# Performance work log

Hardware: AMD Instinct MI355X
Metric: run time of the kernel (lower is better)

## Reference

```python
import jax, jax.numpy as jnp
import numpy as np

B, C, T = 32, 256, 4096

def setup_inputs() -> dict:
    key = jax.random.key(0)
    k1, k2 = jax.random.split(key)
    x = jax.random.normal(k1, (B, C, T), dtype=jnp.float32)
    gamma = jax.random.normal(k2, (1,), dtype=jnp.float32)
    return {"x": x, "gamma": gamma}

def reference(x, gamma):
    # energy[b,i,j] = <x[b,i,:], x[b,j,:]>  -> (B, C, C)
    energy = jnp.einsum('bit,bjt->bij', x, x)
    # max-subtract trick: softmax over (rowmax - energy)
    energy_new = jnp.max(energy, axis=-1, keepdims=True) - energy
    attention = jax.nn.softmax(energy_new, axis=-1)
    # out[b,i,t] = sum_j attention[b,i,j] * x[b,j,t]
    out = jnp.einsum('bij,bjt->bit', attention, x)
    return gamma * out + x
```

## Files before the change

### kernel.cpp

```cpp
#include <hip/hip_runtime.h>
#include <hip/hip_bf16.h>

#define BATCH 32
#define CDIM  256
#define TDIM  4096

using short8  = __attribute__((ext_vector_type(8))) short;
using floatx4 = __attribute__((ext_vector_type(4))) float;

__device__ __forceinline__ unsigned f2bf(float f) {
  unsigned u = __float_as_uint(f);
  return (u + 0x7fffu + ((u >> 16) & 1u)) >> 16;
}
__device__ __forceinline__ unsigned cvt_pk_bf16(float a, float b) {
  return f2bf(a) | (f2bf(b) << 16);
}
__device__ __forceinline__ float bf_lo(unsigned u) { return __uint_as_float(u << 16); }
__device__ __forceinline__ float bf_hi(unsigned u) { return __uint_as_float(u & 0xffff0000u); }

__global__ __launch_bounds__(512, 1)
void gram_kernel(const float* __restrict__ x,
                 float* __restrict__ E1, float* __restrict__ E2) {
  __shared__ __align__(16) short hI[128 * 64];
  __shared__ __align__(16) short lI[128 * 64];
  __shared__ __align__(16) short hJ[64 * 64];

  const int tid = threadIdx.x;
  const int bx  = blockIdx.x;

  const int s   = bx & 7;
  const int seq = bx >> 3;
  const int b   = s + ((seq >> 3) << 3);
  const int job = seq & 7;
  const int i0  = (job >> 2) << 7;
  const int j0  = (job & 3) << 6;

  const float* xb = x + ((size_t)b << 20);

  const bool isJ   = tid >= 256;
  const int  irow  = tid >> 1;
  const int  ihalf = tid & 1;
  const int  jrow  = (tid & 255) >> 2;
  const int  jq    = tid & 3;

  const float* pS = isJ
      ? xb + (size_t)(j0 + jrow) * TDIM + (jq << 4)
      : xb + (size_t)(i0 + irow) * TDIM + (ihalf << 5);

  floatx4 acc1[2][2], acc2[2][2];
#pragma unroll
  for (int m = 0; m < 2; ++m)
#pragma unroll
    for (int n = 0; n < 2; ++n) {
      acc1[m][n] = {0.f, 0.f, 0.f, 0.f};
      acc2[m][n] = {0.f, 0.f, 0.f, 0.f};
    }

  const int lane = tid & 63;
  const int w    = tid >> 6;
  const int wib  = (w >> 1) << 5;
  const int wjb  = (w & 1) << 5;
  const int fr   = lane & 15;
  const int q    = lane >> 4;
  const int f7   = fr & 7;

  const int g0 = ((q)     ^ f7) << 3;
  const int g1 = ((q + 4) ^ f7) << 3;
  const int a0 = (wib + fr) << 6;
  const int a1 = (wib + 16 + fr) << 6;
  const int b0 = (wjb + fr) << 6;
  const int b1 = (wjb + 16 + fr) << 6;

  float4 r0, r1, r2, r3, r4, r5, r6, r7;
  r0 = ((const float4*)pS)[0]; r1 = ((const float4*)pS)[1];
  r2 = ((const float4*)pS)[2]; r3 = ((const float4*)pS)[3];
  if (!isJ) {
    r4 = ((const float4*)pS)[4]; r5 = ((const float4*)pS)[5];
    r6 = ((const float4*)pS)[6]; r7 = ((const float4*)pS)[7];
  }

  for (int ks = 0; ks < TDIM / 64; ++ks) {
    unsigned h0 = cvt_pk_bf16(r0.x, r0.y), h1 = cvt_pk_bf16(r0.z, r0.w);
    unsigned h2 = cvt_pk_bf16(r1.x, r1.y), h3 = cvt_pk_bf16(r1.z, r1.w);
    unsigned h4 = cvt_pk_bf16(r2.x, r2.y), h5 = cvt_pk_bf16(r2.z, r2.w);
    unsigned h6 = cvt_pk_bf16(r3.x, r3.y), h7 = cvt_pk_bf16(r3.z, r3.w);
    unsigned h8, h9, hA, hB, hC, hD, hE, hF;
    unsigned l0, l1, l2, l3, l4, l5, l6, l7, l8, l9, lA, lB, lC, lD, lE, lF;
    if (!isJ) {
      h8 = cvt_pk_bf16(r4.x, r4.y); h9 = cvt_pk_bf16(r4.z, r4.w);
      hA = cvt_pk_bf16(r5.x, r5.y); hB = cvt_pk_bf16(r5.z, r5.w);
      hC = cvt_pk_bf16(r6.x, r6.y); hD = cvt_pk_bf16(r6.z, r6.w);
      hE = cvt_pk_bf16(r7.x, r7.y); hF = cvt_pk_bf16(r7.z, r7.w);
      l0 = cvt_pk_bf16(r0.x - bf_lo(h0), r0.y - bf_hi(h0));
      l1 = cvt_pk_bf16(r0.z - bf_lo(h1), r0.w - bf_hi(h1));
      l2 = cvt_pk_bf16(r1.x - bf_lo(h2), r1.y - bf_hi(h2));
      l3 = cvt_pk_bf16(r1.z - bf_lo(h3), r1.w - bf_hi(h3));
      l4 = cvt_pk_bf16(r2.x - bf_lo(h4), r2.y - bf_hi(h4));
      l5 = cvt_pk_bf16(r2.z - bf_lo(h5), r2.w - bf_hi(h5));
      l6 = cvt_pk_bf16(r3.x - bf_lo(h6), r3.y - bf_hi(h6));
      l7 = cvt_pk_bf16(r3.z - bf_lo(h7), r3.w - bf_hi(h7));
      l8 = cvt_pk_bf16(r4.x - bf_lo(h8), r4.y - bf_hi(h8));
      l9 = cvt_pk_bf16(r4.z - bf_lo(h9), r4.w - bf_hi(h9));
      lA = cvt_pk_bf16(r5.x - bf_lo(hA), r5.y - bf_hi(hA));
      lB = cvt_pk_bf16(r5.z - bf_lo(hB), r5.w - bf_hi(hB));
      lC = cvt_pk_bf16(r6.x - bf_lo(hC), r6.y - bf_hi(hC));
      lD = cvt_pk_bf16(r6.z - bf_lo(hD), r6.w - bf_hi(hD));
      lE = cvt_pk_bf16(r7.x - bf_lo(hE), r7.y - bf_hi(hE));
      lF = cvt_pk_bf16(r7.z - bf_lo(hF), r7.w - bf_hi(hF));
    }

    __syncthreads();
    if (!isJ) {
      const int rb = irow << 6;
      const int s7 = irow & 7;
      const int gb = ihalf << 2;
      *(uint4*)&hI[rb + (((gb + 0) ^ s7) << 3)] = make_uint4(h0, h1, h2, h3);
      *(uint4*)&hI[rb + (((gb + 1) ^ s7) << 3)] = make_uint4(h4, h5, h6, h7);
      *(uint4*)&hI[rb + (((gb + 2) ^ s7) << 3)] = make_uint4(h8, h9, hA, hB);
      *(uint4*)&hI[rb + (((gb + 3) ^ s7) << 3)] = make_uint4(hC, hD, hE, hF);
      *(uint4*)&lI[rb + (((gb + 0) ^ s7) << 3)] = make_uint4(l0, l1, l2, l3);
      *(uint4*)&lI[rb + (((gb + 1) ^ s7) << 3)] = make_uint4(l4, l5, l6, l7);
      *(uint4*)&lI[rb + (((gb + 2) ^ s7) << 3)] = make_uint4(l8, l9, lA, lB);
      *(uint4*)&lI[rb + (((gb + 3) ^ s7) << 3)] = make_uint4(lC, lD, lE, lF);
    } else {
      const int rb = jrow << 6;
      const int s7 = jrow & 7;
      const int gb = jq << 1;
      *(uint4*)&hJ[rb + (((gb + 0) ^ s7) << 3)] = make_uint4(h0, h1, h2, h3);
      *(uint4*)&hJ[rb + (((gb + 1) ^ s7) << 3)] = make_uint4(h4, h5, h6, h7);
    }
    __syncthreads();

    if (ks < TDIM / 64 - 1) {
      pS += 64;
      r0 = ((const float4*)pS)[0]; r1 = ((const float4*)pS)[1];
      r2 = ((const float4*)pS)[2]; r3 = ((const float4*)pS)[3];
      if (!isJ) {
        r4 = ((const float4*)pS)[4]; r5 = ((const float4*)pS)[5];
        r6 = ((const float4*)pS)[6]; r7 = ((const float4*)pS)[7];
      }
    }

    {
      short8 Ah0 = *(const short8*)&hI[a0 + g0];
      short8 Ah1 = *(const short8*)&hI[a1 + g0];
      short8 Al0 = *(const short8*)&lI[a0 + g0];
      short8 Al1 = *(const short8*)&lI[a1 + g0];
      short8 Bh0 = *(const short8*)&hJ[b0 + g0];
      short8 Bh1 = *(const short8*)&hJ[b1 + g0];
      acc1[0][0] = __builtin_amdgcn_mfma_f32_16x16x32_bf16(Ah0, Bh0, acc1[0][0], 0, 0, 0);
      acc1[0][1] = __builtin_amdgcn_mfma_f32_16x16x32_bf16(Ah0, Bh1, acc1[0][1], 0, 0, 0);
      acc1[1][0] = __builtin_amdgcn_mfma_f32_16x16x32_bf16(Ah1, Bh0, acc1[1][0], 0, 0, 0);
      acc1[1][1] = __builtin_amdgcn_mfma_f32_16x16x32_bf16(Ah1, Bh1, acc1[1][1], 0, 0, 0);
      acc2[0][0] = __builtin_amdgcn_mfma_f32_16x16x32_bf16(Al0, Bh0, acc2[0][0], 0, 0, 0);
      acc2[0][1] = __builtin_amdgcn_mfma_f32_16x16x32_bf16(Al0, Bh1, acc2[0][1], 0, 0, 0);
      acc2[1][0] = __builtin_amdgcn_mfma_f32_16x16x32_bf16(Al1, Bh0, acc2[1][0], 0, 0, 0);
      acc2[1][1] = __builtin_amdgcn_mfma_f32_16x16x32_bf16(Al1, Bh1, acc2[1][1], 0, 0, 0);
    }
    {
      short8 Ah0 = *(const short8*)&hI[a0 + g1];
      short8 Ah1 = *(const short8*)&hI[a1 + g1];
      short8 Al0 = *(const short8*)&lI[a0 + g1];
      short8 Al1 = *(const short8*)&lI[a1 + g1];
      short8 Bh0 = *(const short8*)&hJ[b0 + g1];
      short8 Bh1 = *(const short8*)&hJ[b1 + g1];
      acc1[0][0] = __builtin_amdgcn_mfma_f32_16x16x32_bf16(Ah0, Bh0, acc1[0][0], 0, 0, 0);
      acc1[0][1] = __builtin_amdgcn_mfma_f32_16x16x32_bf16(Ah0, Bh1, acc1[0][1], 0, 0, 0);
      acc1[1][0] = __builtin_amdgcn_mfma_f32_16x16x32_bf16(Ah1, Bh0, acc1[1][0], 0, 0, 0);
      acc1[1][1] = __builtin_amdgcn_mfma_f32_16x16x32_bf16(Ah1, Bh1, acc1[1][1], 0, 0, 0);
      acc2[0][0] = __builtin_amdgcn_mfma_f32_16x16x32_bf16(Al0, Bh0, acc2[0][0], 0, 0, 0);
      acc2[0][1] = __builtin_amdgcn_mfma_f32_16x16x32_bf16(Al0, Bh1, acc2[0][1], 0, 0, 0);
      acc2[1][0] = __builtin_amdgcn_mfma_f32_16x16x32_bf16(Al1, Bh0, acc2[1][0], 0, 0, 0);
      acc2[1][1] = __builtin_amdgcn_mfma_f32_16x16x32_bf16(Al1, Bh1, acc2[1][1], 0, 0, 0);
    }
  }

#pragma unroll
  for (int m = 0; m < 2; ++m)
#pragma unroll
    for (int n = 0; n < 2; ++n) {
      const int gr = i0 + wib + 16 * m + 4 * q;
      const int gc = j0 + wjb + 16 * n + fr;
      size_t base = (((size_t)b * CDIM + gr) << 8) + gc;
#pragma unroll
      for (int r = 0; r < 4; ++r) {
        E1[base + ((size_t)r << 8)] = acc1[m][n][r];
        E2[base + ((size_t)r << 8)] = acc2[m][n][r];
      }
    }
}

__global__ __launch_bounds__(256)
void softmax_kernel(const float* __restrict__ E1, const float* __restrict__ E2,
                    __hip_bfloat16* __restrict__ att) {
  __shared__ float SR[32][264];
  __shared__ float ST[256][33];

  const int tid = threadIdx.x;
  const int b   = blockIdx.x >> 3;
  const int i0  = (blockIdx.x & 7) << 5;
  const size_t base = (size_t)b << 16;

  {
    const int r  = tid >> 3;
    const int c0 = (tid & 7) << 5;
    const float* p1 = E1 + base + ((size_t)(i0 + r) << 8) + c0;
    const float* p2 = E2 + base + ((size_t)(i0 + r) << 8) + c0;
#pragma unroll
    for (int u = 0; u < 32; u += 4) {
      float4 a = *(const float4*)(p1 + u);
      float4 c = *(const float4*)(p2 + u);
      *(float4*)&SR[r][c0 + u] = make_float4(a.x + c.x, a.y + c.y, a.z + c.z, a.w + c.w);
    }
  }
  {
    const int c  = tid & 31;
    const int j0 = (tid >> 5) << 5;
    const float* p = E2 + base + i0 + c;
#pragma unroll
    for (int jj = 0; jj < 32; ++jj)
      ST[j0 + jj][c] = p[(size_t)(j0 + jj) << 8];
  }
  __syncthreads();

  const int r  = tid >> 3;
  const int t7 = tid & 7;
  float z[32];
  float m = -3.4e38f;
#pragma unroll
  for (int k = 0; k < 32; ++k) {
    const int j = t7 + (k << 3);
    const float e = SR[r][j] + ST[j][r];
    z[k] = -e;
    m = fmaxf(m, z[k]);
  }
  m = fmaxf(m, __shfl_xor(m, 1, 64));
  m = fmaxf(m, __shfl_xor(m, 2, 64));
  m = fmaxf(m, __shfl_xor(m, 4, 64));
  float ssum = 0.f;
#pragma unroll
  for (int k = 0; k < 32; ++k) { z[k] = expf(z[k] - m); ssum += z[k]; }
  ssum += __shfl_xor(ssum, 1, 64);
  ssum += __shfl_xor(ssum, 2, 64);
  ssum += __shfl_xor(ssum, 4, 64);
  const float inv = 1.f / ssum;

  unsigned short* arow = (unsigned short*)att + base + ((size_t)(i0 + r) << 8);
#pragma unroll
  for (int k = 0; k < 32; ++k) {
    const int j = t7 + (k << 3);
    arow[j] = (unsigned short)f2bf(z[k] * inv);
  }
}

__global__ __launch_bounds__(256, 2)
void pv_kernel(const float* __restrict__ x, const __hip_bfloat16* __restrict__ att,
               const float* __restrict__ gamma, float* __restrict__ out) {
  __shared__ __align__(16) short As[128 * 40];
  __shared__ __align__(16) short Bt[128 * 40];

  const int tid = threadIdx.x;
  const int bx  = blockIdx.x;
  const int b   = bx >> 6;
  const int i0  = ((bx >> 5) & 1) << 7;
  const int t0  = (bx & 31) << 7;

  const float* xb = x + ((size_t)b << 20);
  const unsigned short* attb = (const unsigned short*)att + ((size_t)b << 16);

  const int arow = tid >> 1;
  const int aoff = (tid & 1) << 4;
  const int kg = tid >> 5;
  const int tg = tid & 31;

  floatx4 acc[4][4];
#pragma unroll
  for (int m = 0; m < 4; ++m)
#pragma unroll
    for (int n = 0; n < 4; ++n) acc[m][n] = {0.f, 0.f, 0.f, 0.f};

  const int lane = tid & 63;
  const int w    = tid >> 6;
  const int wm   = (w >> 1) << 6;
  const int wn   = (w & 1) << 6;
  const int fr   = lane & 15;
  const int q    = lane >> 4;

  const unsigned short* pA = attb + (size_t)(i0 + arow) * CDIM + aoff;
  const float* pB = xb + (size_t)(kg * 4) * TDIM + t0 + tg;

  uint4 ra0 = *(const uint4*)pA;
  uint4 ra1 = *(const uint4*)(pA + 8);
  float xv[4][4];
#pragma unroll
  for (int kk = 0; kk < 4; ++kk)
#pragma unroll
    for (int tt = 0; tt < 4; ++tt) xv[kk][tt] = pB[kk * TDIM + tt * 32];

  for (int ks = 0; ks < CDIM / 32; ++ks) {
    unsigned bu[4][2];
#pragma unroll
    for (int tt = 0; tt < 4; ++tt) {
      bu[tt][0] = cvt_pk_bf16(xv[0][tt], xv[1][tt]);
      bu[tt][1] = cvt_pk_bf16(xv[2][tt], xv[3][tt]);
    }

    __syncthreads();
    *(uint4*)(&As[arow * 40 + aoff])     = ra0;
    *(uint4*)(&As[arow * 40 + aoff + 8]) = ra1;
#pragma unroll
    for (int tt = 0; tt < 4; ++tt)
      *(uint2*)(&Bt[(tg + tt * 32) * 40 + kg * 4]) = make_uint2(bu[tt][0], bu[tt][1]);
    __syncthreads();

    if (ks < CDIM / 32 - 1) {
      pA += 32; pB += (size_t)32 * TDIM;
      ra0 = *(const uint4*)pA;
      ra1 = *(const uint4*)(pA + 8);
#pragma unroll
      for (int kk = 0; kk < 4; ++kk)
#pragma unroll
        for (int tt = 0; tt < 4; ++tt) xv[kk][tt] = pB[kk * TDIM + tt * 32];
    }

    short8 Af[4], Bf[4];
#pragma unroll
    for (int m = 0; m < 4; ++m) Af[m] = *(const short8*)(&As[(wm + 16 * m + fr) * 40 + q * 8]);
#pragma unroll
    for (int n = 0; n < 4; ++n) Bf[n] = *(const short8*)(&Bt[(wn + 16 * n + fr) * 40 + q * 8]);
#pragma unroll
    for (int m = 0; m < 4; ++m)
#pragma unroll
      for (int n = 0; n < 4; ++n)
        acc[m][n] = __builtin_amdgcn_mfma_f32_16x16x32_bf16(Af[m], Bf[n], acc[m][n], 0, 0, 0);
  }

  const float g = gamma[0];
#pragma unroll
  for (int m = 0; m < 4; ++m)
#pragma unroll
    for (int n = 0; n < 4; ++n) {
      const int gr = i0 + wm + 16 * m + 4 * q;
      const int gc = t0 + wn + 16 * n + fr;
      size_t base = ((size_t)b << 20) + (size_t)gr * TDIM + gc;
#pragma unroll
      for (int r = 0; r < 4; ++r) {
        size_t idx = base + (size_t)r * TDIM;
        out[idx] = g * acc[m][n][r] + x[idx];
      }
    }
}

extern "C" void kernel_launch(void* const* d_in, const int* in_sizes, int n_in,
                              void* d_out, int out_size, void* d_ws, size_t ws_size,
                              hipStream_t stream) {
  (void)in_sizes; (void)n_in; (void)out_size; (void)ws_size;
  const float* x     = (const float*)d_in[0];
  const float* gamma = (const float*)d_in[1];
  float* out = (float*)d_out;

  const size_t EN = (size_t)BATCH * CDIM * CDIM;
  float* E1 = (float*)d_ws;
  float* E2 = E1 + EN;
  __hip_bfloat16* att = (__hip_bfloat16*)(E2 + EN);

  gram_kernel<<<dim3(256), dim3(512), 0, stream>>>(x, E1, E2);
  softmax_kernel<<<dim3(BATCH * 8), dim3(256), 0, stream>>>(E1, E2, att);
  pv_kernel<<<dim3(2048), dim3(256), 0, stream>>>(x, att, gamma, out);
}
```

Measured before the change: 408.3 us.

## Stage full K extent of attention and x tiles in LDS with XOR swizzle

The PV kernel now loads the whole 128x256 attention tile and the 128x256 bf16 x tile into shared memory up front, using vectorized float4 loads of x and an XOR swizzle to avoid bank conflicts. The per-k-step double barrier loop is replaced by a single barrier followed by a fully unrolled MFMA loop. This removes repeated synchronisation and narrow scalar loads, but uses 128KB of LDS and drops to one block per CU. Global loads are no longer overlapped with compute.

```diff
diff --git a/kernel.cpp b/kernel.cpp
--- a/kernel.cpp
+++ b/kernel.cpp
@@ -253,11 +253,11 @@
   }
 }
 
-__global__ __launch_bounds__(256, 2)
+__global__ __launch_bounds__(256, 1)
 void pv_kernel(const float* __restrict__ x, const __hip_bfloat16* __restrict__ att,
                const float* __restrict__ gamma, float* __restrict__ out) {
-  __shared__ __align__(16) short As[128 * 40];
-  __shared__ __align__(16) short Bt[128 * 40];
+  __shared__ __align__(16) short As[128 * 256];
+  __shared__ __align__(16) short Bs[128 * 256];
 
   const int tid = threadIdx.x;
   const int bx  = blockIdx.x;
@@ -265,13 +265,49 @@
   const int i0  = ((bx >> 5) & 1) << 7;
   const int t0  = (bx & 31) << 7;
 
-  const float* xb = x + ((size_t)b << 20);
-  const unsigned short* attb = (const unsigned short*)att + ((size_t)b << 16);
-
-  const int arow = tid >> 1;
-  const int aoff = (tid & 1) << 4;
-  const int kg = tid >> 5;
-  const int tg = tid & 31;
+  const float* xb = x + ((size_t)b << 20) + t0;
+  const unsigned short* attb =
+      (const unsigned short*)att + ((size_t)b << 16) + ((size_t)i0 << 8);
+
+  {
+    uint4 areg[16];
+#pragma unroll
+    for (int c = 0; c < 16; ++c) {
+      const int p = (c << 8) + tid;
+      const int r = p >> 5;
+      const int g = (p & 31) ^ (r & 7);
+      areg[c] = *(const uint4*)(attb + (r << 8) + (g << 3));
+    }
+#pragma unroll
+    for (int c = 0; c < 16; ++c) {
+      const int p = (c << 8) + tid;
+      *(uint4*)((char*)As + ((size_t)p << 4)) = areg[c];
+    }
+  }
+
+  {
+    const int tQ = tid & 31;
+    const int jg = tid >> 5;
+#pragma unroll
+    for (int j8 = 0; j8 < 4; ++j8) {
+      floatx4 v[8];
+#pragma unroll
+      for (int u = 0; u < 8; ++u) {
+        const int j = (jg << 5) + (j8 << 3) + u;
+        v[u] = *(const floatx4*)(xb + (size_t)j * TDIM + (tQ << 2));
+      }
+#pragma unroll
+      for (int tt = 0; tt < 4; ++tt) {
+        uint4 wv = make_uint4(cvt_pk_bf16(v[0][tt], v[1][tt]),
+                              cvt_pk_bf16(v[2][tt], v[3][tt]),
+                              cvt_pk_bf16(v[4][tt], v[5][tt]),
+                              cvt_pk_bf16(v[6][tt], v[7][tt]));
+        const int row = (tQ << 2) + tt;
+        const int g   = ((jg << 2) + j8) ^ (row & 7);
+        *(uint4*)((char*)Bs + (size_t)row * 512 + ((size_t)g << 4)) = wv;
+      }
+    }
+  }
 
   floatx4 acc[4][4];
 #pragma unroll
@@ -286,48 +322,23 @@
   const int fr   = lane & 15;
   const int q    = lane >> 4;
 
-  const unsigned short* pA = attb + (size_t)(i0 + arow) * CDIM + aoff;
-  const float* pB = xb + (size_t)(kg * 4) * TDIM + t0 + tg;
-
-  uint4 ra0 = *(const uint4*)pA;
-  uint4 ra1 = *(const uint4*)(pA + 8);
-  float xv[4][4];
-#pragma unroll
-  for (int kk = 0; kk < 4; ++kk)
-#pragma unroll
-    for (int tt = 0; tt < 4; ++tt) xv[kk][tt] = pB[kk * TDIM + tt * 32];
-
-  for (int ks = 0; ks < CDIM / 32; ++ks) {
-    unsigned bu[4][2];
-#pragma unroll
-    for (int tt = 0; tt < 4; ++tt) {
-      bu[tt][0] = cvt_pk_bf16(xv[0][tt], xv[1][tt]);
-      bu[tt][1] = cvt_pk_bf16(xv[2][tt], xv[3][tt]);
-    }
-
-    __syncthreads();
-    *(uint4*)(&As[arow * 40 + aoff])     = ra0;
-    *(uint4*)(&As[arow * 40 + aoff + 8]) = ra1;
-#pragma unroll
-    for (int tt = 0; tt < 4; ++tt)
-      *(uint2*)(&Bt[(tg + tt * 32) * 40 + kg * 4]) = make_uint2(bu[tt][0], bu[tt][1]);
-    __syncthreads();
-
-    if (ks < CDIM / 32 - 1) {
-      pA += 32; pB += (size_t)32 * TDIM;
-      ra0 = *(const uint4*)pA;
-      ra1 = *(const uint4*)(pA + 8);
-#pragma unroll
-      for (int kk = 0; kk < 4; ++kk)
-#pragma unroll
-        for (int tt = 0; tt < 4; ++tt) xv[kk][tt] = pB[kk * TDIM + tt * 32];
-    }
-
+  __syncthreads();
+
+#pragma unroll
+  for (int ks = 0; ks < 8; ++ks) {
     short8 Af[4], Bf[4];
 #pragma unroll
-    for (int m = 0; m < 4; ++m) Af[m] = *(const short8*)(&As[(wm + 16 * m + fr) * 40 + q * 8]);
-#pragma unroll
-    for (int n = 0; n < 4; ++n) Bf[n] = *(const short8*)(&Bt[(wn + 16 * n + fr) * 40 + q * 8]);
+    for (int m = 0; m < 4; ++m) {
+      const int r = wm + 16 * m + fr;
+      const int g = ((ks << 2) + q) ^ (r & 7);
+      Af[m] = *(const short8*)((char*)As + (size_t)r * 512 + ((size_t)g << 4));
+    }
+#pragma unroll
+    for (int n = 0; n < 4; ++n) {
+      const int r = wn + 16 * n + fr;
+      const int g = ((ks << 2) + q) ^ (r & 7);
+      Bf[n] = *(const short8*)((char*)Bs + (size_t)r * 512 + ((size_t)g << 4));
+    }
 #pragma unroll
     for (int m = 0; m < 4; ++m)
 #pragma unroll
```

Result: faster. 400.0 us (-2.0%).
